# Kernel optimization log

Measured on AMD Instinct MI355X. Metric: run time of the kernel, lower is better.

The kernel has to match this reference:

```python
import jax, jax.numpy as jnp
import numpy as np

D = 256          # hidden_dim
H = 4            # num_heads
HD = D // H      # head_dim = 64
E = 4            # num_experts (hard-coded in MoE)
TOPK = 2         # top_k (hard-coded)
DFF = 2 * D      # expert ffn width
EPS = 1e-5


def _ln(x, g, b):
    mu = x.mean(-1, keepdims=True)
    var = x.var(-1, keepdims=True)  # biased, matches torch LayerNorm
    return (x - mu) * jax.lax.rsqrt(var + EPS) * g + b


def _ff(x, w1, b1, w2, b2):
    h = jax.nn.gelu(x @ w1 + b1, approximate=False)  # torch nn.GELU default = exact erf
    return h @ w2 + b2


def setup_inputs() -> dict:
    key = jax.random.key(0)
    ks = jax.random.split(key, 24)
    B, S, IN = 4, 2048, 256
    s = 0.02
    inp = {
        'x': jax.random.normal(ks[0], (B, S, IN), jnp.float32),
        'mask': jax.random.randint(ks[1], (B, S), 0, 2).astype(jnp.int32),
        'w_in': jax.random.normal(ks[2], (IN, D), jnp.float32) * s,
        'b_in': jnp.zeros((D,), jnp.float32),
        'g1': jnp.ones((D,), jnp.float32),
        'be1': jnp.zeros((D,), jnp.float32),
        'wq': jax.random.normal(ks[3], (D, D), jnp.float32) * s,
        'bq': jnp.zeros((D,), jnp.float32),
        'wk': jax.random.normal(ks[4], (D, D), jnp.float32) * s,
        'bk': jnp.zeros((D,), jnp.float32),
        'wv': jax.random.normal(ks[5], (D, D), jnp.float32) * s,
        'bv': jnp.zeros((D,), jnp.float32),
        'wo': jax.random.normal(ks[6], (D, D), jnp.float32) * s,
        'bo': jnp.zeros((D,), jnp.float32),
        'g2': jnp.ones((D,), jnp.float32),
        'be2': jnp.zeros((D,), jnp.float32),
        'wg': jax.random.normal(ks[7], (D, E), jnp.float32) * s,
        'bg': jnp.zeros((E,), jnp.float32),
        'ew1': jax.random.normal(ks[8], (E, D, DFF), jnp.float32) * s,
        'eb1': jnp.zeros((E, DFF), jnp.float32),
        'ew2': jax.random.normal(ks[9], (E, DFF, D), jnp.float32) * s,
        'eb2': jnp.zeros((E, D), jnp.float32),
    }
    return inp


def reference(x, mask, w_in, b_in, g1, be1, wq, bq, wk, bk, wv, bv, wo, bo, g2, be2, wg, bg, ew1, eb1, ew2, eb2):
    B, S, _ = x.shape
    x = x @ w_in + b_in
    res = x
    h = _ln(x, g1, be1)
    q = (h @ wq + bq).reshape(B, S, H, HD).transpose(0, 2, 1, 3)  # bhsd
    k = (h @ wk + bk).reshape(B, S, H, HD).transpose(0, 2, 1, 3)
    v = (h @ wv + bv).reshape(B, S, H, HD).transpose(0, 2, 1, 3)
    # RoPE (interleaved pairs, half-concat output, as in source)
    inv_freq = 1.0 / (10000.0 ** (jnp.arange(0, HD, 2, dtype=jnp.float32) / HD))
    ang = jnp.arange(S, dtype=jnp.float32)[:, None] * inv_freq[None, :]  # [S, HD//2]
    sin, cos = jnp.sin(ang), jnp.cos(ang)  # broadcast over (B,H)
    def rot(t):
        ts = t.reshape(B, H, S, HD // 2, 2)
        t0, t1 = ts[..., 0], ts[..., 1]
        return jnp.concatenate([t0 * cos - t1 * sin, t1 * cos + t0 * sin], axis=-1)
    qr, kr = rot(q), rot(k)
    attn = jnp.einsum('bhqd,bhkd->bhqk', qr, kr) * (HD ** -0.5)
    row = mask[:, None, :, None]  # [B,1,S,1] -> masks whole query rows
    attn = jnp.where(row == 0, jnp.float32(-1e4), attn)
    valid = (row * S).astype(jnp.float32)           # [B,1,S,1]
    all_masked = valid == 0
    uniform = jnp.where(row != 0, 1.0 / jnp.maximum(valid, 1.0), 0.0)
    attn = jnp.where(all_masked, uniform, attn)
    attn = jax.nn.softmax(attn, axis=-1)
    out = jnp.einsum('bhqk,bhkd->bhqd', attn, v).transpose(0, 2, 1, 3).reshape(B, S, D)
    out = out @ wo + bo
    x = res + out
    res2 = x
    h2 = _ln(x, g2, be2)
    # MoE (faithful: expert i only applied where top-k slot i picked expert i)
    gp = jax.nn.softmax(h2 @ wg + bg, axis=-1)
    topv, topi = jax.lax.top_k(gp, TOPK)
    moe_out = jnp.zeros_like(h2)
    for i in range(TOPK):
        eo = _ff(h2, ew1[i], eb1[i], ew2[i], eb2[i])
        m = (topi[..., i] == i)[..., None].astype(h2.dtype)
        moe_out = moe_out + m * eo * topv[..., i:i + 1]
    flat = topi.reshape(-1)
    total = sum((flat == i).sum() for i in range(TOPK)).astype(jnp.float32)
    usage = jnp.zeros((E,), jnp.float32) + total
    usage = usage / usage.sum()
    lb = (jnp.std(usage, ddof=1) / usage.mean()) ** 2
    y = res2 + h2  # source discards moe_out / lb (likely a bug); kept live with exact 0* add
    return y + 0.0 * (moe_out.sum() + lb)
```

## Files before the change

kernel.cpp:

```cpp
#include <hip/hip_runtime.h>
#include <cstddef>

#define Bb    4
#define Sq    2048
#define Dd    256
#define Hh    4
#define HDh   64
#define NROWS (Bb*Sq)
#define EPSf  1e-5f

typedef unsigned short u16;
typedef unsigned int   u32;
typedef unsigned long long u64;
typedef __attribute__((ext_vector_type(8))) short  frag_ab;
typedef __attribute__((ext_vector_type(4))) float  frag_cd;

__device__ __forceinline__ u16 f2bf(float f){
    union { float f; u32 u; } v; v.f = f;
    u32 r = v.u + 0x7fffu + ((v.u >> 16) & 1u);
    return (u16)(r >> 16);
}
__device__ __forceinline__ u16 f2bf_trunc(float f){
    union { float f; u32 u; } v; v.f = f;
    return (u16)(v.u >> 16);
}
__device__ __forceinline__ float bf2f(u32 u){
    union { u32 u; float f; } v; v.u = u << 16; return v.f;
}

__global__ __launch_bounds__(256) void k0_prep(
    const float* __restrict__ w_in, const float* __restrict__ wq,
    const float* __restrict__ wk,   const float* __restrict__ wv,
    const float* __restrict__ wo,
    u16* __restrict__ wT, float* __restrict__ tab)
{
    const int bid = blockIdx.x, tid = threadIdx.x;
    if (bid < 80){
        __shared__ float T[64][65];
        const int wsel = bid >> 4, tile = bid & 15;
        const int k0 = (tile >> 2) * 64, n0 = (tile & 3) * 64;
        const float* src = wsel==0 ? w_in : wsel==1 ? wq : wsel==2 ? wk
                         : wsel==3 ? wv : wo;
        #pragma unroll
        for (int i=0;i<16;++i){
            int idx = i*256 + tid, k = idx>>6, n = idx&63;
            T[k][n] = src[(size_t)(k0+k)*Dd + n0 + n];
        }
        __syncthreads();
        u16* dst = wT + (size_t)wsel*Dd*Dd;
        #pragma unroll
        for (int i=0;i<16;++i){
            int idx = i*256 + tid, n = idx>>6, k = idx&63;
            dst[(size_t)(n0+n)*Dd + k0 + k] = f2bf(T[k][n]);
        }
    } else {
        int s = (bid-80)*8 + (tid>>5);
        int p = tid & 31;
        float invf = exp2f(-(float)p * (13.287712379549449f/32.f));
        float sn, cs; sincosf((float)s * invf, &sn, &cs);
        tab[(size_t)s*64 + p]      = cs;
        tab[(size_t)s*64 + 32 + p] = sn;
    }
}

__global__ __launch_bounds__(256) void k1_fused(
    const float* __restrict__ x,  const float* __restrict__ tab,
    const u16* __restrict__ wTin, const u16* __restrict__ wTq,
    const u16* __restrict__ wTk,  const u16* __restrict__ wTv,
    const float* __restrict__ b_in, const float* __restrict__ g1,
    const float* __restrict__ be1,  const float* __restrict__ bq,
    const float* __restrict__ bk,   const float* __restrict__ bv,
    float* __restrict__ x1, u16* __restrict__ qro,
    u16* __restrict__ kro,  u16* __restrict__ vto)
{
    const int tid  = threadIdx.x;
    const int w    = tid >> 6;
    const int lane = tid & 63;
    const int l16  = lane & 15;
    const int quad = lane >> 4;
    const int r0   = blockIdx.x * 32;
    const int b    = r0 >> 11;
    const int s0   = r0 & (Sq-1);
    const int cb   = w * 64;
    const int c4   = cb + quad*4;

    __shared__ u16 Xs[32][264];
    __shared__ u16 Hs[32][264];
    __shared__ u16 Os[32][264];
    __shared__ float red[2][32][4];

    #pragma unroll
    for (int i=0;i<8;++i){
        int f = i*256 + tid;
        int row = f>>6, cc = f&63;
        float4 v4 = *(const float4*)(x + (size_t)(r0+row)*Dd + cc*4);
        u16 pk4[4] = { f2bf(v4.x), f2bf(v4.y), f2bf(v4.z), f2bf(v4.w) };
        *(u64*)&Xs[row][cc*4] = *(u64*)pk4;
    }
    __syncthreads();

    frag_cd acc[2][4];
    #pragma unroll
    for (int nt=0;nt<4;++nt){
        float4 b4 = *(const float4*)&b_in[c4 + nt*16];
        acc[0][nt] = (frag_cd){b4.x, b4.y, b4.z, b4.w};
        acc[1][nt] = acc[0][nt];
    }
    #pragma unroll
    for (int kc=0;kc<8;++kc){
        frag_ab xa0 = *(frag_ab*)&Xs[l16][kc*32 + quad*8];
        frag_ab xa1 = *(frag_ab*)&Xs[16+l16][kc*32 + quad*8];
        #pragma unroll
        for (int nt=0;nt<4;++nt){
            frag_ab wf = *(const frag_ab*)&wTin[(size_t)(cb+nt*16+l16)*Dd + kc*32 + quad*8];
            acc[0][nt] = __builtin_amdgcn_mfma_f32_16x16x32_bf16(wf, xa0, acc[0][nt], 0,0,0);
            acc[1][nt] = __builtin_amdgcn_mfma_f32_16x16x32_bf16(wf, xa1, acc[1][nt], 0,0,0);
        }
    }

    #pragma unroll
    for (int rg=0;rg<2;++rg){
        float s=0.f, q=0.f;
        #pragma unroll
        for (int nt=0;nt<4;++nt){
            float4 v4 = make_float4(acc[rg][nt][0], acc[rg][nt][1],
                                    acc[rg][nt][2], acc[rg][nt][3]);
            *(float4*)&x1[(size_t)(r0+rg*16+l16)*Dd + c4 + nt*16] = v4;
            s += v4.x+v4.y+v4.z+v4.w;
            q += v4.x*v4.x + v4.y*v4.y + v4.z*v4.z + v4.w*v4.w;
        }
        s += __shfl_xor(s,16); q += __shfl_xor(q,16);
        s += __shfl_xor(s,32); q += __shfl_xor(q,32);
        if (lane < 16){ red[0][rg*16+l16][w]=s; red[1][rg*16+l16][w]=q; }
    }
    __syncthreads();

    #pragma unroll
    for (int rg=0;rg<2;++rg){
        int row = rg*16 + l16;
        float mu = (red[0][row][0]+red[0][row][1]+red[0][row][2]+red[0][row][3])*(1.f/Dd);
        float ms = (red[1][row][0]+red[1][row][1]+red[1][row][2]+red[1][row][3])*(1.f/Dd);
        float rstd = rsqrtf(ms - mu*mu + EPSf);
        #pragma unroll
        for (int nt=0;nt<4;++nt){
            float4 g4 = *(const float4*)&g1[c4 + nt*16];
            float4 e4 = *(const float4*)&be1[c4 + nt*16];
            u16 pk4[4] = { f2bf((acc[rg][nt][0]-mu)*rstd*g4.x + e4.x),
                           f2bf((acc[rg][nt][1]-mu)*rstd*g4.y + e4.y),
                           f2bf((acc[rg][nt][2]-mu)*rstd*g4.z + e4.z),
                           f2bf((acc[rg][nt][3]-mu)*rstd*g4.w + e4.w) };
            *(u64*)&Hs[row][c4 + nt*16] = *(u64*)pk4;
        }
    }
    __syncthreads();

    const u16*   wps[3] = { wTq, wTk, wTv };
    const float* bps[3] = { bq, bk, bv };
    #pragma unroll
    for (int tt=0; tt<3; ++tt){
        frag_cd a2[2][4];
        #pragma unroll
        for (int nt=0;nt<4;++nt){
            float4 b4 = *(const float4*)&bps[tt][c4 + nt*16];
            a2[0][nt] = (frag_cd){b4.x, b4.y, b4.z, b4.w};
            a2[1][nt] = a2[0][nt];
        }
        #pragma unroll
        for (int kc=0;kc<8;++kc){
            frag_ab ha0 = *(frag_ab*)&Hs[l16][kc*32 + quad*8];
            frag_ab ha1 = *(frag_ab*)&Hs[16+l16][kc*32 + quad*8];
            #pragma unroll
            for (int nt=0;nt<4;++nt){
                frag_ab wf = *(const frag_ab*)&wps[tt][(size_t)(cb+nt*16+l16)*Dd + kc*32 + quad*8];
                a2[0][nt] = __builtin_amdgcn_mfma_f32_16x16x32_bf16(wf, ha0, a2[0][nt], 0,0,0);
                a2[1][nt] = __builtin_amdgcn_mfma_f32_16x16x32_bf16(wf, ha1, a2[1][nt], 0,0,0);
            }
        }
        #pragma unroll
        for (int rg=0;rg<2;++rg)
            #pragma unroll
            for (int nt=0;nt<4;++nt){
                u16 pk4[4] = { f2bf(a2[rg][nt][0]), f2bf(a2[rg][nt][1]),
                               f2bf(a2[rg][nt][2]), f2bf(a2[rg][nt][3]) };
                *(u64*)&Os[rg*16+l16][c4 + nt*16] = *(u64*)pk4;
            }
        __syncthreads();

        if (tt < 2){
            #pragma unroll
            for (int rg=0;rg<2;++rg){
                const int row  = rg*16 + (tid >> 4);
                const int head = (tid >> 2) & 3;
                const int pq   = tid & 3;
                const int sidx = s0 + row;
                const float* tb = tab + (size_t)sidx*64;
                float4 c0 = *(const float4*)(tb + pq*8);
                float4 c1 = *(const float4*)(tb + pq*8 + 4);
                float4 sn0 = *(const float4*)(tb + 32 + pq*8);
                float4 sn1 = *(const float4*)(tb + 32 + pq*8 + 4);
                const float cA[8] = {c0.x,c0.y,c0.z,c0.w,c1.x,c1.y,c1.z,c1.w};
                const float sA[8] = {sn0.x,sn0.y,sn0.z,sn0.w,sn1.x,sn1.y,sn1.z,sn1.w};
                u16* dst = (tt==0 ? qro : kro) + ((size_t)(b*Hh+head)*Sq + sidx)*HDh;
                u16 lo[8], hi[8];
                #pragma unroll
                for (int j=0;j<8;++j){
                    int p = pq*8 + j;
                    u32 pr = *(const u32*)&Os[row][head*64 + 2*p];
                    float t0 = bf2f(pr & 0xffffu), t1 = bf2f(pr >> 16);
                    lo[j] = f2bf(t0*cA[j] - t1*sA[j]);
                    hi[j] = f2bf(t1*cA[j] + t0*sA[j]);
                }
                *(float4*)(dst + pq*8)      = *(float4*)lo;
                *(float4*)(dst + 32 + pq*8) = *(float4*)hi;
            }
        } else {
            const int head = tid >> 6, d = lane;
            #pragma unroll
            for (int rg=0;rg<2;++rg){
                u16 pk[16];
                #pragma unroll
                for (int j=0;j<16;++j) pk[j] = Os[rg*16+j][head*64 + d];
                u16* dst = vto + ((size_t)(b*Hh+head)*HDh + d)*Sq + s0 + rg*16;
                *(float4*)dst     = *(float4*)pk;
                *(float4*)(dst+8) = *(float4*)&pk[8];
            }
        }
        __syncthreads();
    }
}

__global__ __launch_bounds__(512) void k2_attn(
    const u16* __restrict__ qr, const u16* __restrict__ kr,
    const u16* __restrict__ vt, const int* __restrict__ mask,
    u16* __restrict__ Opart, float* __restrict__ lpart)
{
    const int tid = threadIdx.x;
    const int w   = tid >> 6;
    const int lane= tid & 63;
    const int l16 = lane & 15;
    const int quad= lane >> 4;
    const int qt  = blockIdx.x;
    const int bh  = blockIdx.y;
    const int ks  = blockIdx.z;
    const int b   = bh >> 2;
    const int q0  = qt * 128;

    __shared__ u16 Ks [64][72];
    __shared__ u16 Vts[64][72];
    __shared__ u16 Ps [8][16][72];

    const u16* qg = qr + ((size_t)bh*Sq + q0 + w*16 + l16)*HDh;
    frag_ab qf0 = *(const frag_ab*)(qg + quad*8);
    frag_ab qf1 = *(const frag_ab*)(qg + quad*8 + 32);

    const float mf2 = (mask[(size_t)b*Sq + q0 + w*16 + l16] != 0)
                    ? 0.125f*1.44269504f : 0.f;

    float lsum = 0.f;
    frag_cd O[4];
    #pragma unroll
    for (int d=0; d<4; ++d) O[d] = (frag_cd){0.f,0.f,0.f,0.f};

    const u16* kg0 = kr + ((size_t)bh*Sq + ks*512)*HDh;
    const u16* vg0 = vt + (size_t)bh*HDh*Sq + ks*512;

    const int srow = tid >> 3, spart = tid & 7;

    for (int kt=0; kt<8; ++kt){
        __syncthreads();
        const u16* kg = kg0 + (size_t)kt*64*HDh;
        const u16* vg = vg0 + kt*64;
        *(float4*)&Ks [srow][spart*8] = *(const float4*)(kg + srow*HDh + spart*8);
        *(float4*)&Vts[srow][spart*8] = *(const float4*)(vg + (size_t)srow*Sq + spart*8);
        __syncthreads();

        frag_cd sc[4];
        #pragma unroll
        for (int t=0;t<4;++t){
            frag_ab kf0 = *(frag_ab*)&Ks[t*16 + l16][quad*8];
            frag_ab kf1 = *(frag_ab*)&Ks[t*16 + l16][quad*8 + 32];
            frag_cd z = (frag_cd){0.f,0.f,0.f,0.f};
            z = __builtin_amdgcn_mfma_f32_16x16x32_bf16(kf0, qf0, z, 0,0,0);
            z = __builtin_amdgcn_mfma_f32_16x16x32_bf16(kf1, qf1, z, 0,0,0);
            sc[t] = z;
        }

        #pragma unroll
        for (int t=0;t<4;++t){
            float p0 = exp2f(sc[t][0]*mf2);
            float p1 = exp2f(sc[t][1]*mf2);
            float p2 = exp2f(sc[t][2]*mf2);
            float p3 = exp2f(sc[t][3]*mf2);
            lsum += p0+p1+p2+p3;
            u16 pk4[4] = { f2bf_trunc(p0), f2bf_trunc(p1),
                           f2bf_trunc(p2), f2bf_trunc(p3) };
            *(u64*)&Ps[w][l16][t*16 + quad*4] = *(u64*)pk4;
        }

        frag_ab pf0 = *(frag_ab*)&Ps[w][l16][quad*8];
        frag_ab pf1 = *(frag_ab*)&Ps[w][l16][quad*8 + 32];

        #pragma unroll
        for (int d=0; d<4; ++d){
            frag_ab vf0 = *(frag_ab*)&Vts[d*16 + l16][quad*8];
            frag_ab vf1 = *(frag_ab*)&Vts[d*16 + l16][quad*8 + 32];
            O[d] = __builtin_amdgcn_mfma_f32_16x16x32_bf16(vf0, pf0, O[d], 0,0,0);
            O[d] = __builtin_amdgcn_mfma_f32_16x16x32_bf16(vf1, pf1, O[d], 0,0,0);
        }
    }

    u16* Ob = Opart + (((size_t)ks*16 + bh)*Sq + q0 + w*16 + l16)*HDh;
    #pragma unroll
    for (int dt=0; dt<4; ++dt){
        u16 pk4[4] = { f2bf(O[dt][0]), f2bf(O[dt][1]),
                       f2bf(O[dt][2]), f2bf(O[dt][3]) };
        *(u64*)(Ob + dt*16 + quad*4) = *(u64*)pk4;
    }
    lsum += __shfl_xor(lsum,16);
    lsum += __shfl_xor(lsum,32);
    if (lane < 16)
        lpart[((size_t)ks*16 + bh)*Sq + q0 + w*16 + l16] = lsum;
}

__global__ __launch_bounds__(256) void k3_gemm_ln(
    const u16* __restrict__ Opart, const float* __restrict__ lpart,
    const u16* __restrict__ wTo,
    const float* __restrict__ bo, const float* __restrict__ x1,
    const float* __restrict__ g2, const float* __restrict__ be2,
    float* __restrict__ out)
{
    const int tid  = threadIdx.x;
    const int w    = tid >> 6;
    const int lane = tid & 63;
    const int l16  = lane & 15;
    const int quad = lane >> 4;
    const int r0   = blockIdx.x * 32;
    const int b    = r0 >> 11;
    const int s0   = r0 & (Sq-1);
    const int cb   = w * 64;
    const int c4   = cb + quad*4;

    __shared__ u16 Ats[32][264];
    __shared__ float red[2][32][4];
    __shared__ float linv[4][32];

    const size_t LS = (size_t)16*Sq;
    if (tid < 128){
        int h = tid >> 5, r = tid & 31;
        size_t li = ((size_t)(b*Hh + h))*Sq + s0 + r;
        linv[h][r] = 1.f / (lpart[li] + lpart[LS + li]
                          + lpart[2*LS + li] + lpart[3*LS + li]);
    }
    __syncthreads();

    const size_t SPLIT = (size_t)16*Sq*HDh;
    #pragma unroll
    for (int i=0;i<8;++i){
        int idx = i*256 + tid;
        int h = idx >> 9, rem = idx & 511, row = rem >> 4, c = rem & 15;
        size_t base = (((size_t)(b*Hh + h))*Sq + s0 + row)*HDh + c*4;
        u64 p0 = *(const u64*)(Opart + base);
        u64 p1 = *(const u64*)(Opart + SPLIT + base);
        u64 p2 = *(const u64*)(Opart + 2*SPLIT + base);
        u64 p3 = *(const u64*)(Opart + 3*SPLIT + base);
        float li = linv[h][row];
        u16 pk[4];
        #pragma unroll
        for (int j=0;j<4;++j){
            float v = bf2f((u32)((p0 >> (16*j)) & 0xffffu))
                    + bf2f((u32)((p1 >> (16*j)) & 0xffffu))
                    + bf2f((u32)((p2 >> (16*j)) & 0xffffu))
                    + bf2f((u32)((p3 >> (16*j)) & 0xffffu));
            pk[j] = f2bf(v*li);
        }
        *(u64*)&Ats[row][h*64 + c*4] = *(u64*)pk;
    }
    __syncthreads();

    frag_cd acc[2][4];
    #pragma unroll
    for (int nt=0;nt<4;++nt){
        float4 b4 = *(const float4*)&bo[c4 + nt*16];
        acc[0][nt] = (frag_cd){b4.x, b4.y, b4.z, b4.w};
        acc[1][nt] = acc[0][nt];
    }
    #pragma unroll
    for (int kc=0;kc<8;++kc){
        frag_ab aa0 = *(frag_ab*)&Ats[l16][kc*32 + quad*8];
        frag_ab aa1 = *(frag_ab*)&Ats[16+l16][kc*32 + quad*8];
        #pragma unroll
        for (int nt=0;nt<4;++nt){
            frag_ab wf = *(const frag_ab*)&wTo[(size_t)(cb+nt*16+l16)*Dd + kc*32 + quad*8];
            acc[0][nt] = __builtin_amdgcn_mfma_f32_16x16x32_bf16(wf, aa0, acc[0][nt], 0,0,0);
            acc[1][nt] = __builtin_amdgcn_mfma_f32_16x16x32_bf16(wf, aa1, acc[1][nt], 0,0,0);
        }
    }

    #pragma unroll
    for (int rg=0;rg<2;++rg){
        float s=0.f, q=0.f;
        #pragma unroll
        for (int nt=0;nt<4;++nt){
            float4 r4 = *(const float4*)&x1[(size_t)(r0+rg*16+l16)*Dd + c4 + nt*16];
            acc[rg][nt][0] += r4.x; acc[rg][nt][1] += r4.y;
            acc[rg][nt][2] += r4.z; acc[rg][nt][3] += r4.w;
            s += acc[rg][nt][0]+acc[rg][nt][1]+acc[rg][nt][2]+acc[rg][nt][3];
            q += acc[rg][nt][0]*acc[rg][nt][0] + acc[rg][nt][1]*acc[rg][nt][1]
               + acc[rg][nt][2]*acc[rg][nt][2] + acc[rg][nt][3]*acc[rg][nt][3];
        }
        s += __shfl_xor(s,16); q += __shfl_xor(q,16);
        s += __shfl_xor(s,32); q += __shfl_xor(q,32);
        if (lane < 16){ red[0][rg*16+l16][w]=s; red[1][rg*16+l16][w]=q; }
    }
    __syncthreads();

    #pragma unroll
    for (int rg=0;rg<2;++rg){
        int row = rg*16 + l16;
        float mu = (red[0][row][0]+red[0][row][1]+red[0][row][2]+red[0][row][3])*(1.f/Dd);
        float ms = (red[1][row][0]+red[1][row][1]+red[1][row][2]+red[1][row][3])*(1.f/Dd);
        float rstd = rsqrtf(ms - mu*mu + EPSf);
        #pragma unroll
        for (int nt=0;nt<4;++nt){
            float4 g4 = *(const float4*)&g2[c4 + nt*16];
            float4 e4 = *(const float4*)&be2[c4 + nt*16];
            float4 o4;
            o4.x = acc[rg][nt][0] + (acc[rg][nt][0]-mu)*rstd*g4.x + e4.x;
            o4.y = acc[rg][nt][1] + (acc[rg][nt][1]-mu)*rstd*g4.y + e4.y;
            o4.z = acc[rg][nt][2] + (acc[rg][nt][2]-mu)*rstd*g4.z + e4.z;
            o4.w = acc[rg][nt][3] + (acc[rg][nt][3]-mu)*rstd*g4.w + e4.w;
            *(float4*)&out[(size_t)(r0+row)*Dd + c4 + nt*16] = o4;
        }
    }
}

extern "C" void kernel_launch(void* const* d_in, const int* in_sizes, int n_in,
                              void* d_out, int out_size, void* d_ws, size_t ws_size,
                              hipStream_t stream)
{
    const float* x    = (const float*)d_in[0];
    const int*   mask = (const int*)  d_in[1];
    const float* w_in = (const float*)d_in[2];
    const float* b_in = (const float*)d_in[3];
    const float* g1   = (const float*)d_in[4];
    const float* be1  = (const float*)d_in[5];
    const float* wq   = (const float*)d_in[6];
    const float* bq   = (const float*)d_in[7];
    const float* wk   = (const float*)d_in[8];
    const float* bk   = (const float*)d_in[9];
    const float* wv   = (const float*)d_in[10];
    const float* bv   = (const float*)d_in[11];
    const float* wo   = (const float*)d_in[12];
    const float* bo   = (const float*)d_in[13];
    const float* g2   = (const float*)d_in[14];
    const float* be2  = (const float*)d_in[15];

    float* out = (float*)d_out;
    char*  wsb = (char*)d_ws;

    float* x1    = (float*)(wsb);
    float* tab   = (float*)(wsb + ( 8u<<20));
    u16*   qro   = (u16*)(wsb + (12u<<20));
    u16*   kro   = (u16*)(wsb + (16u<<20));
    u16*   vto   = (u16*)(wsb + (20u<<20));
    u16*   Opart = (u16*)(wsb + (24u<<20));
    float* lpart = (float*)(wsb + (40u<<20));
    u16*   wT    = (u16*)(wsb + (40u<<20) + (768u<<10));

    k0_prep<<<336, 256, 0, stream>>>(w_in, wq, wk, wv, wo, wT, tab);
    k1_fused<<<NROWS/32, 256, 0, stream>>>(
        x, tab, wT, wT + Dd*Dd, wT + 2*Dd*Dd, wT + 3*Dd*Dd,
        b_in, g1, be1, bq, bk, bv, x1, qro, kro, vto);
    k2_attn<<<dim3(Sq/128, Bb*Hh, 4), 512, 0, stream>>>(qro, kro, vto, mask, Opart, lpart);
    k3_gemm_ln<<<NROWS/32, 256, 0, stream>>>(Opart, lpart, wT + 4*Dd*Dd,
                                             bo, x1, g2, be2, out);
}
```

Before: 178.2 us.

## Use 8 waves per block in k1/k3 and fuse QKV into one GEMM pass

```diff
diff --git a/kernel.cpp b/kernel.cpp
--- a/kernel.cpp
+++ b/kernel.cpp
@@ -63,10 +63,9 @@
     }
 }
 
-__global__ __launch_bounds__(256) void k1_fused(
+__global__ __launch_bounds__(512) void k1_fused(
     const float* __restrict__ x,  const float* __restrict__ tab,
-    const u16* __restrict__ wTin, const u16* __restrict__ wTq,
-    const u16* __restrict__ wTk,  const u16* __restrict__ wTv,
+    const u16* __restrict__ wTin, const u16* __restrict__ wTqkv,
     const float* __restrict__ b_in, const float* __restrict__ g1,
     const float* __restrict__ be1,  const float* __restrict__ bq,
     const float* __restrict__ bk,   const float* __restrict__ bv,
@@ -81,17 +80,15 @@
     const int r0   = blockIdx.x * 32;
     const int b    = r0 >> 11;
     const int s0   = r0 & (Sq-1);
-    const int cb   = w * 64;
-    const int c4   = cb + quad*4;
 
     __shared__ u16 Xs[32][264];
     __shared__ u16 Hs[32][264];
-    __shared__ u16 Os[32][264];
-    __shared__ float red[2][32][4];
-
-    #pragma unroll
-    for (int i=0;i<8;++i){
-        int f = i*256 + tid;
+    __shared__ u16 Os[32][776];
+    __shared__ float red[2][32][8];
+
+    #pragma unroll
+    for (int i=0;i<4;++i){
+        int f = i*512 + tid;
         int row = f>>6, cc = f&63;
         float4 v4 = *(const float4*)(x + (size_t)(r0+row)*Dd + cc*4);
         u16 pk4[4] = { f2bf(v4.x), f2bf(v4.y), f2bf(v4.z), f2bf(v4.w) };
@@ -99,10 +96,11 @@
     }
     __syncthreads();
 
-    frag_cd acc[2][4];
-    #pragma unroll
-    for (int nt=0;nt<4;++nt){
-        float4 b4 = *(const float4*)&b_in[c4 + nt*16];
+    const int cA = w*32 + quad*4;
+    frag_cd acc[2][2];
+    #pragma unroll
+    for (int nt=0;nt<2;++nt){
+        float4 b4 = *(const float4*)&b_in[cA + nt*16];
         acc[0][nt] = (frag_cd){b4.x, b4.y, b4.z, b4.w};
         acc[1][nt] = acc[0][nt];
     }
@@ -111,8 +109,8 @@
         frag_ab xa0 = *(frag_ab*)&Xs[l16][kc*32 + quad*8];
         frag_ab xa1 = *(frag_ab*)&Xs[16+l16][kc*32 + quad*8];
         #pragma unroll
-        for (int nt=0;nt<4;++nt){
-            frag_ab wf = *(const frag_ab*)&wTin[(size_t)(cb+nt*16+l16)*Dd + kc*32 + quad*8];
+        for (int nt=0;nt<2;++nt){
+            frag_ab wf = *(const frag_ab*)&wTin[(size_t)(w*32+nt*16+l16)*Dd + kc*32 + quad*8];
             acc[0][nt] = __builtin_amdgcn_mfma_f32_16x16x32_bf16(wf, xa0, acc[0][nt], 0,0,0);
             acc[1][nt] = __builtin_amdgcn_mfma_f32_16x16x32_bf16(wf, xa1, acc[1][nt], 0,0,0);
         }
@@ -122,10 +120,10 @@
     for (int rg=0;rg<2;++rg){
         float s=0.f, q=0.f;
         #pragma unroll
-        for (int nt=0;nt<4;++nt){
+        for (int nt=0;nt<2;++nt){
             float4 v4 = make_float4(acc[rg][nt][0], acc[rg][nt][1],
                                     acc[rg][nt][2], acc[rg][nt][3]);
-            *(float4*)&x1[(size_t)(r0+rg*16+l16)*Dd + c4 + nt*16] = v4;
+            *(float4*)&x1[(size_t)(r0+rg*16+l16)*Dd + cA + nt*16] = v4;
             s += v4.x+v4.y+v4.z+v4.w;
             q += v4.x*v4.x + v4.y*v4.y + v4.z*v4.z + v4.w*v4.w;
         }
@@ -138,94 +136,92 @@
     #pragma unroll
     for (int rg=0;rg<2;++rg){
         int row = rg*16 + l16;
-        float mu = (red[0][row][0]+red[0][row][1]+red[0][row][2]+red[0][row][3])*(1.f/Dd);
-        float ms = (red[1][row][0]+red[1][row][1]+red[1][row][2]+red[1][row][3])*(1.f/Dd);
+        float s8=0.f, q8=0.f;
+        #pragma unroll
+        for (int j=0;j<8;++j){ s8 += red[0][row][j]; q8 += red[1][row][j]; }
+        float mu = s8*(1.f/Dd), ms = q8*(1.f/Dd);
         float rstd = rsqrtf(ms - mu*mu + EPSf);
         #pragma unroll
-        for (int nt=0;nt<4;++nt){
-            float4 g4 = *(const float4*)&g1[c4 + nt*16];
-            float4 e4 = *(const float4*)&be1[c4 + nt*16];
+        for (int nt=0;nt<2;++nt){
+            float4 g4 = *(const float4*)&g1[cA + nt*16];
+            float4 e4 = *(const float4*)&be1[cA + nt*16];
             u16 pk4[4] = { f2bf((acc[rg][nt][0]-mu)*rstd*g4.x + e4.x),
                            f2bf((acc[rg][nt][1]-mu)*rstd*g4.y + e4.y),
                            f2bf((acc[rg][nt][2]-mu)*rstd*g4.z + e4.z),
                            f2bf((acc[rg][nt][3]-mu)*rstd*g4.w + e4.w) };
-            *(u64*)&Hs[row][c4 + nt*16] = *(u64*)pk4;
-        }
-    }
-    __syncthreads();
-
-    const u16*   wps[3] = { wTq, wTk, wTv };
-    const float* bps[3] = { bq, bk, bv };
-    #pragma unroll
-    for (int tt=0; tt<3; ++tt){
-        frag_cd a2[2][4];
-        #pragma unroll
-        for (int nt=0;nt<4;++nt){
-            float4 b4 = *(const float4*)&bps[tt][c4 + nt*16];
-            a2[0][nt] = (frag_cd){b4.x, b4.y, b4.z, b4.w};
-            a2[1][nt] = a2[0][nt];
-        }
-        #pragma unroll
-        for (int kc=0;kc<8;++kc){
-            frag_ab ha0 = *(frag_ab*)&Hs[l16][kc*32 + quad*8];
-            frag_ab ha1 = *(frag_ab*)&Hs[16+l16][kc*32 + quad*8];
+            *(u64*)&Hs[rg*16+l16][cA + nt*16] = *(u64*)pk4;
+        }
+    }
+    __syncthreads();
+
+    frag_cd a2[2][6];
+    #pragma unroll
+    for (int nt=0;nt<6;++nt){
+        int c0 = w*96 + nt*16;
+        const float* bp = (c0 < 256) ? bq : (c0 < 512 ? bk : bv);
+        int cc = (c0 & 255) + quad*4;
+        float4 b4 = *(const float4*)&bp[cc];
+        a2[0][nt] = (frag_cd){b4.x, b4.y, b4.z, b4.w};
+        a2[1][nt] = a2[0][nt];
+    }
+    #pragma unroll
+    for (int kc=0;kc<8;++kc){
+        frag_ab ha0 = *(frag_ab*)&Hs[l16][kc*32 + quad*8];
+        frag_ab ha1 = *(frag_ab*)&Hs[16+l16][kc*32 + quad*8];
+        #pragma unroll
+        for (int nt=0;nt<6;++nt){
+            frag_ab wf = *(const frag_ab*)&wTqkv[(size_t)(w*96+nt*16+l16)*Dd + kc*32 + quad*8];
+            a2[0][nt] = __builtin_amdgcn_mfma_f32_16x16x32_bf16(wf, ha0, a2[0][nt], 0,0,0);
+            a2[1][nt] = __builtin_amdgcn_mfma_f32_16x16x32_bf16(wf, ha1, a2[1][nt], 0,0,0);
+        }
+    }
+    #pragma unroll
+    for (int rg=0;rg<2;++rg)
+        #pragma unroll
+        for (int nt=0;nt<6;++nt){
+            u16 pk4[4] = { f2bf(a2[rg][nt][0]), f2bf(a2[rg][nt][1]),
+                           f2bf(a2[rg][nt][2]), f2bf(a2[rg][nt][3]) };
+            *(u64*)&Os[rg*16+l16][w*96 + nt*16 + quad*4] = *(u64*)pk4;
+        }
+    __syncthreads();
+
+    {
+        const int row  = tid >> 4;
+        const int head = (tid >> 2) & 3;
+        const int pq   = tid & 3;
+        const int sidx = s0 + row;
+        const float* tb = tab + (size_t)sidx*64;
+        float4 c0 = *(const float4*)(tb + pq*8);
+        float4 c1 = *(const float4*)(tb + pq*8 + 4);
+        float4 sn0 = *(const float4*)(tb + 32 + pq*8);
+        float4 sn1 = *(const float4*)(tb + 32 + pq*8 + 4);
+        const float cAr[8] = {c0.x,c0.y,c0.z,c0.w,c1.x,c1.y,c1.z,c1.w};
+        const float sAr[8] = {sn0.x,sn0.y,sn0.z,sn0.w,sn1.x,sn1.y,sn1.z,sn1.w};
+        #pragma unroll
+        for (int tt=0; tt<2; ++tt){
+            const int cbase = tt*256 + head*64;
+            u16* dst = (tt==0 ? qro : kro) + ((size_t)(b*Hh+head)*Sq + sidx)*HDh;
+            u16 lo[8], hi[8];
             #pragma unroll
-            for (int nt=0;nt<4;++nt){
-                frag_ab wf = *(const frag_ab*)&wps[tt][(size_t)(cb+nt*16+l16)*Dd + kc*32 + quad*8];
-                a2[0][nt] = __builtin_amdgcn_mfma_f32_16x16x32_bf16(wf, ha0, a2[0][nt], 0,0,0);
-                a2[1][nt] = __builtin_amdgcn_mfma_f32_16x16x32_bf16(wf, ha1, a2[1][nt], 0,0,0);
+            for (int j=0;j<8;++j){
+                int p = pq*8 + j;
+                u32 pr = *(const u32*)&Os[row][cbase + 2*p];
+                float t0 = bf2f(pr & 0xffffu), t1 = bf2f(pr >> 16);
+                lo[j] = f2bf(t0*cAr[j] - t1*sAr[j]);
+                hi[j] = f2bf(t1*cAr[j] + t0*sAr[j]);
             }
-        }
-        #pragma unroll
-        for (int rg=0;rg<2;++rg)
-            #pragma unroll
-            for (int nt=0;nt<4;++nt){
-                u16 pk4[4] = { f2bf(a2[rg][nt][0]), f2bf(a2[rg][nt][1]),
-                               f2bf(a2[rg][nt][2]), f2bf(a2[rg][nt][3]) };
-                *(u64*)&Os[rg*16+l16][c4 + nt*16] = *(u64*)pk4;
-            }
-        __syncthreads();
-
-        if (tt < 2){
-            #pragma unroll
-            for (int rg=0;rg<2;++rg){
-                const int row  = rg*16 + (tid >> 4);
-                const int head = (tid >> 2) & 3;
-                const int pq   = tid & 3;
-                const int sidx = s0 + row;
-                const float* tb = tab + (size_t)sidx*64;
-                float4 c0 = *(const float4*)(tb + pq*8);
-                float4 c1 = *(const float4*)(tb + pq*8 + 4);
-                float4 sn0 = *(const float4*)(tb + 32 + pq*8);
-                float4 sn1 = *(const float4*)(tb + 32 + pq*8 + 4);
-                const float cA[8] = {c0.x,c0.y,c0.z,c0.w,c1.x,c1.y,c1.z,c1.w};
-                const float sA[8] = {sn0.x,sn0.y,sn0.z,sn0.w,sn1.x,sn1.y,sn1.z,sn1.w};
-                u16* dst = (tt==0 ? qro : kro) + ((size_t)(b*Hh+head)*Sq + sidx)*HDh;
-                u16 lo[8], hi[8];
-                #pragma unroll
-                for (int j=0;j<8;++j){
-                    int p = pq*8 + j;
-                    u32 pr = *(const u32*)&Os[row][head*64 + 2*p];
-                    float t0 = bf2f(pr & 0xffffu), t1 = bf2f(pr >> 16);
-                    lo[j] = f2bf(t0*cA[j] - t1*sA[j]);
-                    hi[j] = f2bf(t1*cA[j] + t0*sA[j]);
-                }
-                *(float4*)(dst + pq*8)      = *(float4*)lo;
-                *(float4*)(dst + 32 + pq*8) = *(float4*)hi;
-            }
-        } else {
-            const int head = tid >> 6, d = lane;
-            #pragma unroll
-            for (int rg=0;rg<2;++rg){
-                u16 pk[16];
-                #pragma unroll
-                for (int j=0;j<16;++j) pk[j] = Os[rg*16+j][head*64 + d];
-                u16* dst = vto + ((size_t)(b*Hh+head)*HDh + d)*Sq + s0 + rg*16;
-                *(float4*)dst     = *(float4*)pk;
-                *(float4*)(dst+8) = *(float4*)&pk[8];
-            }
-        }
-        __syncthreads();
+            *(float4*)(dst + pq*8)      = *(float4*)lo;
+            *(float4*)(dst + 32 + pq*8) = *(float4*)hi;
+        }
+    }
+    {
+        const int head = tid >> 7, d = (tid >> 1) & 63, rg = tid & 1;
+        u16 pk[16];
+        #pragma unroll
+        for (int j=0;j<16;++j) pk[j] = Os[rg*16+j][512 + head*64 + d];
+        u16* dst = vto + ((size_t)(b*Hh+head)*HDh + d)*Sq + s0 + rg*16;
+        *(float4*)dst     = *(float4*)pk;
+        *(float4*)(dst+8) = *(float4*)&pk[8];
     }
 }
 
@@ -322,7 +318,7 @@
         lpart[((size_t)ks*16 + bh)*Sq + q0 + w*16 + l16] = lsum;
 }
 
-__global__ __launch_bounds__(256) void k3_gemm_ln(
+__global__ __launch_bounds__(512) void k3_gemm_ln(
     const u16* __restrict__ Opart, const float* __restrict__ lpart,
     const u16* __restrict__ wTo,
     const float* __restrict__ bo, const float* __restrict__ x1,
@@ -337,11 +333,10 @@
     const int r0   = blockIdx.x * 32;
     const int b    = r0 >> 11;
     const int s0   = r0 & (Sq-1);
-    const int cb   = w * 64;
-    const int c4   = cb + quad*4;
+    const int cA   = w*32 + quad*4;
 
     __shared__ u16 Ats[32][264];
-    __shared__ float red[2][32][4];
+    __shared__ float red[2][32][8];
     __shared__ float linv[4][32];
 
     const size_t LS = (size_t)16*Sq;
@@ -355,8 +350,8 @@
 
     const size_t SPLIT = (size_t)16*Sq*HDh;
     #pragma unroll
-    for (int i=0;i<8;++i){
-        int idx = i*256 + tid;
+    for (int i=0;i<4;++i){
+        int idx = i*512 + tid;
         int h = idx >> 9, rem = idx & 511, row = rem >> 4, c = rem & 15;
         size_t base = (((size_t)(b*Hh + h))*Sq + s0 + row)*HDh + c*4;
         u64 p0 = *(const u64*)(Opart + base);
@@ -377,10 +372,10 @@
     }
     __syncthreads();
 
-    frag_cd acc[2][4];
-    #pragma unroll
-    for (int nt=0;nt<4;++nt){
-        float4 b4 = *(const float4*)&bo[c4 + nt*16];
+    frag_cd acc[2][2];
+    #pragma unroll
+    for (int nt=0;nt<2;++nt){
+        float4 b4 = *(const float4*)&bo[cA + nt*16];
         acc[0][nt] = (frag_cd){b4.x, b4.y, b4.z, b4.w};
         acc[1][nt] = acc[0][nt];
     }
@@ -389,8 +384,8 @@
         frag_ab aa0 = *(frag_ab*)&Ats[l16][kc*32 + quad*8];
         frag_ab aa1 = *(frag_ab*)&Ats[16+l16][kc*32 + quad*8];
         #pragma unroll
-        for (int nt=0;nt<4;++nt){
-            frag_ab wf = *(const frag_ab*)&wTo[(size_t)(cb+nt*16+l16)*Dd + kc*32 + quad*8];
+        for (int nt=0;nt<2;++nt){
+            frag_ab wf = *(const frag_ab*)&wTo[(size_t)(w*32+nt*16+l16)*Dd + kc*32 + quad*8];
             acc[0][nt] = __builtin_amdgcn_mfma_f32_16x16x32_bf16(wf, aa0, acc[0][nt], 0,0,0);
             acc[1][nt] = __builtin_amdgcn_mfma_f32_16x16x32_bf16(wf, aa1, acc[1][nt], 0,0,0);
         }
@@ -400,8 +395,8 @@
     for (int rg=0;rg<2;++rg){
         float s=0.f, q=0.f;
         #pragma unroll
-        for (int nt=0;nt<4;++nt){
-            float4 r4 = *(const float4*)&x1[(size_t)(r0+rg*16+l16)*Dd + c4 + nt*16];
+        for (int nt=0;nt<2;++nt){
+            float4 r4 = *(const float4*)&x1[(size_t)(r0+rg*16+l16)*Dd + cA + nt*16];
             acc[rg][nt][0] += r4.x; acc[rg][nt][1] += r4.y;
             acc[rg][nt][2] += r4.z; acc[rg][nt][3] += r4.w;
             s += acc[rg][nt][0]+acc[rg][nt][1]+acc[rg][nt][2]+acc[rg][nt][3];
@@ -417,19 +412,21 @@
     #pragma unroll
     for (int rg=0;rg<2;++rg){
         int row = rg*16 + l16;
-        float mu = (red[0][row][0]+red[0][row][1]+red[0][row][2]+red[0][row][3])*(1.f/Dd);
-        float ms = (red[1][row][0]+red[1][row][1]+red[1][row][2]+red[1][row][3])*(1.f/Dd);
+        float s8=0.f, q8=0.f;
+        #pragma unroll
+        for (int j=0;j<8;++j){ s8 += red[0][row][j]; q8 += red[1][row][j]; }
+        float mu = s8*(1.f/Dd), ms = q8*(1.f/Dd);
         float rstd = rsqrtf(ms - mu*mu + EPSf);
         #pragma unroll
-        for (int nt=0;nt<4;++nt){
-            float4 g4 = *(const float4*)&g2[c4 + nt*16];
-            float4 e4 = *(const float4*)&be2[c4 + nt*16];
+        for (int nt=0;nt<2;++nt){
+            float4 g4 = *(const float4*)&g2[cA + nt*16];
+            float4 e4 = *(const float4*)&be2[cA + nt*16];
             float4 o4;
             o4.x = acc[rg][nt][0] + (acc[rg][nt][0]-mu)*rstd*g4.x + e4.x;
             o4.y = acc[rg][nt][1] + (acc[rg][nt][1]-mu)*rstd*g4.y + e4.y;
             o4.z = acc[rg][nt][2] + (acc[rg][nt][2]-mu)*rstd*g4.z + e4.z;
             o4.w = acc[rg][nt][3] + (acc[rg][nt][3]-mu)*rstd*g4.w + e4.w;
-            *(float4*)&out[(size_t)(r0+row)*Dd + c4 + nt*16] = o4;
+            *(float4*)&out[(size_t)(r0+row)*Dd + cA + nt*16] = o4;
         }
     }
 }
@@ -468,10 +465,10 @@
     u16*   wT    = (u16*)(wsb + (40u<<20) + (768u<<10));
 
     k0_prep<<<336, 256, 0, stream>>>(w_in, wq, wk, wv, wo, wT, tab);
-    k1_fused<<<NROWS/32, 256, 0, stream>>>(
-        x, tab, wT, wT + Dd*Dd, wT + 2*Dd*Dd, wT + 3*Dd*Dd,
+    k1_fused<<<NROWS/32, 512, 0, stream>>>(
+        x, tab, wT, wT + Dd*Dd,
         b_in, g1, be1, bq, bk, bv, x1, qro, kro, vto);
     k2_attn<<<dim3(Sq/128, Bb*Hh, 4), 512, 0, stream>>>(qro, kro, vto, mask, Opart, lpart);
-    k3_gemm_ln<<<NROWS/32, 256, 0, stream>>>(Opart, lpart, wT + 4*Dd*Dd,
+    k3_gemm_ln<<<NROWS/32, 512, 0, stream>>>(Opart, lpart, wT + 4*Dd*Dd,
                                              bo, x1, g2, be2, out);
 }
```

Result: faster. 170.7 us (-4.2%).
